# Kernel optimization log

Hardware: AMD Instinct MI355X
Metric: run time of the kernel (lower is better)

## Reference

```python
import jax, jax.numpy as jnp
import numpy as np

HIDDEN = 128
STATE = 256
SEQ = 4096
BATCH = 16


def _op(q_i, q_j):
    # Binary operator for the parallel scan of the 2x2 block-diagonal recurrence.
    # m: (..., 4, N) holding [A, B, C, D] blocks; f: (..., 2, N) holding [b1, b2].
    m_i, f_i = q_i
    m_j, f_j = q_j
    iA, iB, iC, iD = m_i[..., 0, :], m_i[..., 1, :], m_i[..., 2, :], m_i[..., 3, :]
    jA, jB, jC, jD = m_j[..., 0, :], m_j[..., 1, :], m_j[..., 2, :], m_j[..., 3, :]
    m_new = jnp.stack([
        jA * iA + jB * iC,
        jA * iB + jB * iD,
        jC * iA + jD * iC,
        jC * iB + jD * iD,
    ], axis=-2)
    b1, b2 = f_i[..., 0, :], f_i[..., 1, :]
    f_new = jnp.stack([jA * b1 + jB * b2, jC * b1 + jD * b2], axis=-2) + f_j
    return m_new, f_new


def _apply_linoss_im(A_diag, B, x, step):
    # x: (L, H); B: (N, H); A_diag, step: (N,)
    Bu = x @ B.T                                    # (L, N)
    s2A = step ** 2 * A_diag
    schur = 1.0 / (1.0 + s2A)
    M11 = 1.0 - s2A * schur
    M12 = -step * A_diag * schur
    M21 = step * schur
    M22 = schur
    L, N = x.shape[0], A_diag.shape[0]
    M = jnp.broadcast_to(jnp.stack([M11, M12, M21, M22]), (L, 4, N))  # (L, 4, N)
    F = jnp.stack([M11 * Bu * step, M21 * Bu * step], axis=1)          # (L, 2, N)
    _, xs = jax.lax.associative_scan(_op, (M, F))
    return xs[:, 1, :]  # second state component y_k, shape (L, N)


def setup_inputs() -> dict:
    key = jax.random.key(0)
    kx, kA, ks, kB, kC, kD = jax.random.split(key, 6)
    x = jax.random.normal(kx, (BATCH, SEQ, HIDDEN), dtype=jnp.float32)
    A_diag = jax.random.uniform(kA, (STATE,), dtype=jnp.float32)
    steps = 0.5 * jax.random.normal(ks, (STATE,), dtype=jnp.float32)
    B = jax.random.normal(kB, (STATE, HIDDEN), dtype=jnp.float32) / np.sqrt(HIDDEN)
    C = jax.random.normal(kC, (HIDDEN, STATE), dtype=jnp.float32) / np.sqrt(STATE)
    D = jax.random.normal(kD, (HIDDEN,), dtype=jnp.float32)
    return {"x": x, "A_diag": A_diag, "steps": steps, "B": B, "C": C, "D": D}


def reference(x, A_diag, steps, B, C, D):
    # Parameter projections used by the mixer (LinOSS-IM, non-damped):
    step = jax.nn.sigmoid(steps)
    A = jax.nn.relu(A_diag)

    def per_seq(xs):
        ys = _apply_linoss_im(A, B, xs, step)   # (L, N)
        return ys @ C.T + D * xs                # (L, H)

    return jax.vmap(per_seq)(x)  # (B, L, H)
```

## Files before the change

### kernel.cpp

```cpp
#include <hip/hip_runtime.h>
#include <hip/hip_bf16.h>

#define BATCHN 16
#define SEQ 4096
#define HIDDEN 128
#define STATE 256
#define MTOT (BATCHN*SEQ)
#define NCHUNK 64
#define LCHUNK 64

typedef __bf16 bf16;
typedef __bf16 bf16x4 __attribute__((ext_vector_type(4)));
typedef __bf16 bf16x8 __attribute__((ext_vector_type(8)));
typedef float f32x4 __attribute__((ext_vector_type(4)));

__global__ __launch_bounds__(256) void setup_k(const float* __restrict__ A_diag,
        const float* __restrict__ steps, const float* __restrict__ Bm,
        const float* __restrict__ Cm, bf16* __restrict__ Bbf, bf16* __restrict__ Cbf,
        float* __restrict__ prm) {
    int idx = blockIdx.x * 256 + threadIdx.x;
    if (idx < STATE * HIDDEN) {
        Bbf[idx] = (bf16)Bm[idx];
        Cbf[idx] = (bf16)Cm[idx];
    }
    if (blockIdx.x == 0) {
        int n = threadIdx.x;
        float st = 1.0f / (1.0f + expf(-steps[n]));
        float A  = fmaxf(A_diag[n], 0.0f);
        float s2A = st * st * A;
        float schur = 1.0f / (1.0f + s2A);
        float m11 = 1.0f - s2A * schur;
        float m12 = -st * A * schur;
        float m21 = st * schur;
        float m22 = schur;
        prm[0*STATE+n] = m11;
        prm[1*STATE+n] = m12;
        prm[2*STATE+n] = m21;
        prm[3*STATE+n] = m22;
        prm[4*STATE+n] = m11 * st;
        prm[5*STATE+n] = m21 * st;
    }
}

__device__ __forceinline__ void stage_x(const float* __restrict__ x, int m0, int tid,
                                        bf16 (*xl)[136]) {
    #pragma unroll
    for (int p = 0; p < 8; ++p) {
        int flat = p * 256 + tid;
        int row = flat >> 5;
        int c4  = flat & 31;
        float4 v = *reinterpret_cast<const float4*>(&x[(size_t)(m0 + row) * HIDDEN + c4 * 4]);
        bf16x4 w = { (bf16)v.x, (bf16)v.y, (bf16)v.z, (bf16)v.w };
        *reinterpret_cast<bf16x4*>(&xl[row][c4 * 4]) = w;
    }
}

__device__ __forceinline__ void gemm1_to_lds(const bf16 (*xl)[136],
        const bf16* __restrict__ Bbf, int tid, bf16 (*bu)[264]) {
    const int wid = tid >> 6, lane = tid & 63;
    const int lr = lane & 15;
    const int lk = (lane >> 4) * 8;
    const int n0 = wid * 64;
    f32x4 acc[4][4];
    #pragma unroll
    for (int i = 0; i < 4; ++i)
        #pragma unroll
        for (int j = 0; j < 4; ++j) acc[i][j] = f32x4{0.f, 0.f, 0.f, 0.f};
    #pragma unroll
    for (int ks = 0; ks < 4; ++ks) {
        int k = ks * 32 + lk;
        bf16x8 a[4], b[4];
        #pragma unroll
        for (int mf = 0; mf < 4; ++mf)
            a[mf] = *reinterpret_cast<const bf16x8*>(&xl[mf * 16 + lr][k]);
        #pragma unroll
        for (int nf = 0; nf < 4; ++nf)
            b[nf] = *reinterpret_cast<const bf16x8*>(&Bbf[(size_t)(n0 + nf * 16 + lr) * HIDDEN + k]);
        #pragma unroll
        for (int mf = 0; mf < 4; ++mf)
            #pragma unroll
            for (int nf = 0; nf < 4; ++nf)
                acc[mf][nf] = __builtin_amdgcn_mfma_f32_16x16x32_bf16(a[mf], b[nf], acc[mf][nf], 0, 0, 0);
    }
    const int mrow = (lane >> 4) * 4;
    #pragma unroll
    for (int mf = 0; mf < 4; ++mf)
        #pragma unroll
        for (int nf = 0; nf < 4; ++nf)
            #pragma unroll
            for (int r = 0; r < 4; ++r)
                bu[mf * 16 + mrow + r][n0 + nf * 16 + lr] = (bf16)acc[mf][nf][r];
}

__global__ __launch_bounds__(256) void k1_gemm_scanA(const float* __restrict__ x,
        const bf16* __restrict__ Bbf, const float* __restrict__ prm,
        float* __restrict__ cs) {
    __shared__ bf16 xl[64][136];
    __shared__ bf16 bu[64][264];
    const int tid = threadIdx.x;
    const int m0 = blockIdx.x * 64;
    stage_x(x, m0, tid, xl);
    __syncthreads();
    gemm1_to_lds(xl, Bbf, tid, bu);
    __syncthreads();
    const int n = tid;
    const float m11 = prm[n], m12 = prm[STATE + n], m21 = prm[2*STATE + n],
                m22 = prm[3*STATE + n], c1 = prm[4*STATE + n], c2 = prm[5*STATE + n];
    float s1 = 0.f, s2 = 0.f;
    #pragma unroll 8
    for (int t = 0; t < LCHUNK; ++t) {
        float v = (float)bu[t][n];
        float ns1 = fmaf(m11, s1, fmaf(m12, s2, c1 * v));
        float ns2 = fmaf(m21, s1, fmaf(m22, s2, c2 * v));
        s1 = ns1; s2 = ns2;
    }
    const int b = m0 >> 12;
    const int chunk = (m0 >> 6) & (NCHUNK - 1);
    size_t base = ((size_t)(b * NCHUNK + chunk) * 2) * STATE + n;
    cs[base] = s1;
    cs[base + STATE] = s2;
}

__global__ __launch_bounds__(256) void scan_comb(float* __restrict__ cs,
        const float* __restrict__ prm) {
    const int n = threadIdx.x;
    const int b = blockIdx.x;
    float p11 = prm[n], p12 = prm[STATE + n], p21 = prm[2*STATE + n], p22 = prm[3*STATE + n];
    #pragma unroll
    for (int i = 0; i < 6; ++i) {
        float q11 = p11 * p11 + p12 * p21;
        float q12 = p11 * p12 + p12 * p22;
        float q21 = p21 * p11 + p22 * p21;
        float q22 = p21 * p12 + p22 * p22;
        p11 = q11; p12 = q12; p21 = q21; p22 = q22;
    }
    float S1 = 0.f, S2 = 0.f;
    #pragma unroll 8
    for (int c = 0; c < NCHUNK; ++c) {
        size_t base = ((size_t)(b * NCHUNK + c) * 2) * STATE + n;
        float q1 = cs[base], q2 = cs[base + STATE];
        cs[base] = S1; cs[base + STATE] = S2;
        float n1 = fmaf(p11, S1, fmaf(p12, S2, q1));
        float n2 = fmaf(p21, S1, fmaf(p22, S2, q2));
        S1 = n1; S2 = n2;
    }
}

__global__ __launch_bounds__(256) void k2_gemm_scan_gemm(const float* __restrict__ x,
        const bf16* __restrict__ Bbf, const bf16* __restrict__ Cbf,
        const float* __restrict__ prm, const float* __restrict__ cs,
        const float* __restrict__ Dv, float* __restrict__ out) {
    __shared__ bf16 xl[64][136];
    __shared__ bf16 bu[64][264];
    const int tid = threadIdx.x;
    const int m0 = blockIdx.x * 64;
    stage_x(x, m0, tid, xl);
    __syncthreads();
    gemm1_to_lds(xl, Bbf, tid, bu);
    __syncthreads();
    {
        const int n = tid;
        const float m11 = prm[n], m12 = prm[STATE + n], m21 = prm[2*STATE + n],
                    m22 = prm[3*STATE + n], c1 = prm[4*STATE + n], c2 = prm[5*STATE + n];
        const int b = m0 >> 12;
        const int chunk = (m0 >> 6) & (NCHUNK - 1);
        size_t cbase = ((size_t)(b * NCHUNK + chunk) * 2) * STATE + n;
        float s1 = cs[cbase], s2 = cs[cbase + STATE];
        #pragma unroll 8
        for (int t = 0; t < LCHUNK; ++t) {
            float v = (float)bu[t][n];
            float ns1 = fmaf(m11, s1, fmaf(m12, s2, c1 * v));
            float ns2 = fmaf(m21, s1, fmaf(m22, s2, c2 * v));
            s1 = ns1; s2 = ns2;
            bu[t][n] = (bf16)s2;
        }
    }
    __syncthreads();
    const int wid = tid >> 6, lane = tid & 63;
    const int lr = lane & 15;
    const int lk = (lane >> 4) * 8;
    const int h0 = wid * 32;
    f32x4 acc2[4][2];
    #pragma unroll
    for (int i = 0; i < 4; ++i) {
        acc2[i][0] = f32x4{0.f, 0.f, 0.f, 0.f};
        acc2[i][1] = f32x4{0.f, 0.f, 0.f, 0.f};
    }
    #pragma unroll
    for (int ks = 0; ks < 8; ++ks) {
        int k = ks * 32 + lk;
        bf16x8 a[4], bb[2];
        #pragma unroll
        for (int mf = 0; mf < 4; ++mf)
            a[mf] = *reinterpret_cast<const bf16x8*>(&bu[mf * 16 + lr][k]);
        #pragma unroll
        for (int hf = 0; hf < 2; ++hf)
            bb[hf] = *reinterpret_cast<const bf16x8*>(&Cbf[(size_t)(h0 + hf * 16 + lr) * STATE + k]);
        #pragma unroll
        for (int mf = 0; mf < 4; ++mf)
            #pragma unroll
            for (int hf = 0; hf < 2; ++hf)
                acc2[mf][hf] = __builtin_amdgcn_mfma_f32_16x16x32_bf16(a[mf], bb[hf], acc2[mf][hf], 0, 0, 0);
    }
    const int mrow = (lane >> 4) * 4;
    #pragma unroll
    for (int mf = 0; mf < 4; ++mf)
        #pragma unroll
        for (int hf = 0; hf < 2; ++hf) {
            int h = h0 + hf * 16 + lr;
            float d = Dv[h];
            #pragma unroll
            for (int r = 0; r < 4; ++r) {
                int ml = mf * 16 + mrow + r;
                out[(size_t)(m0 + ml) * HIDDEN + h] = acc2[mf][hf][r] + d * (float)xl[ml][h];
            }
        }
}

extern "C" void kernel_launch(void* const* d_in, const int* in_sizes, int n_in,
                              void* d_out, int out_size, void* d_ws, size_t ws_size,
                              hipStream_t stream) {
    const float* x      = (const float*)d_in[0];
    const float* A_diag = (const float*)d_in[1];
    const float* steps  = (const float*)d_in[2];
    const float* Bm     = (const float*)d_in[3];
    const float* Cm     = (const float*)d_in[4];
    const float* Dv     = (const float*)d_in[5];
    float* out = (float*)d_out;

    char* ws = (char*)d_ws;
    const size_t CS_BYTES = (size_t)BATCHN * NCHUNK * 2 * STATE * 4;
    float* cs  = (float*)ws;
    bf16*  Bbf = (bf16*)(ws + CS_BYTES);
    bf16*  Cbf = (bf16*)(ws + CS_BYTES + (size_t)STATE * HIDDEN * 2);
    float* prm = (float*)(ws + CS_BYTES + (size_t)STATE * HIDDEN * 4);

    hipLaunchKernelGGL(setup_k, dim3(128), dim3(256), 0, stream, A_diag, steps, Bm, Cm, Bbf, Cbf, prm);
    hipLaunchKernelGGL(k1_gemm_scanA, dim3(MTOT / 64), dim3(256), 0, stream, x, Bbf, prm, cs);
    hipLaunchKernelGGL(scan_comb, dim3(BATCHN), dim3(256), 0, stream, cs, prm);
    hipLaunchKernelGGL(k2_gemm_scan_gemm, dim3(MTOT / 64), dim3(256), 0, stream,
                       x, Bbf, Cbf, prm, cs, Dv, out);
}
```

Measured before the change: 56.93 us.

## Drop setup kernel, preload B/C fragments into registers, coalesce output stores

Removes the setup kernel by recomputing the scan parameters inline in each kernel. Weight fragments are now loaded straight from fp32 B and C into registers before the main work, so they are no longer read from global inside the GEMM loops. The output epilogue is staged through LDS so the D*x add and the global store use coalesced float4 writes. Launch bounds now request 3 blocks per SM. The trade-offs are higher register pressure, redundant weight conversion in every block, and an extra LDS round trip.

```diff
diff --git a/kernel.cpp b/kernel.cpp
--- a/kernel.cpp
+++ b/kernel.cpp
@@ -14,32 +14,27 @@
 typedef __bf16 bf16x8 __attribute__((ext_vector_type(8)));
 typedef float f32x4 __attribute__((ext_vector_type(4)));
 
-__global__ __launch_bounds__(256) void setup_k(const float* __restrict__ A_diag,
-        const float* __restrict__ steps, const float* __restrict__ Bm,
-        const float* __restrict__ Cm, bf16* __restrict__ Bbf, bf16* __restrict__ Cbf,
-        float* __restrict__ prm) {
-    int idx = blockIdx.x * 256 + threadIdx.x;
-    if (idx < STATE * HIDDEN) {
-        Bbf[idx] = (bf16)Bm[idx];
-        Cbf[idx] = (bf16)Cm[idx];
-    }
-    if (blockIdx.x == 0) {
-        int n = threadIdx.x;
-        float st = 1.0f / (1.0f + expf(-steps[n]));
-        float A  = fmaxf(A_diag[n], 0.0f);
-        float s2A = st * st * A;
-        float schur = 1.0f / (1.0f + s2A);
-        float m11 = 1.0f - s2A * schur;
-        float m12 = -st * A * schur;
-        float m21 = st * schur;
-        float m22 = schur;
-        prm[0*STATE+n] = m11;
-        prm[1*STATE+n] = m12;
-        prm[2*STATE+n] = m21;
-        prm[3*STATE+n] = m22;
-        prm[4*STATE+n] = m11 * st;
-        prm[5*STATE+n] = m21 * st;
-    }
+__device__ __forceinline__ void scan_params(const float* __restrict__ A_diag,
+        const float* __restrict__ steps, int n,
+        float& m11, float& m12, float& m21, float& m22, float& c1, float& c2) {
+    float st = 1.0f / (1.0f + expf(-steps[n]));
+    float A  = fmaxf(A_diag[n], 0.0f);
+    float s2A = st * st * A;
+    float schur = 1.0f / (1.0f + s2A);
+    m11 = 1.0f - s2A * schur;
+    m12 = -st * A * schur;
+    m21 = st * schur;
+    m22 = schur;
+    c1 = m11 * st;
+    c2 = m21 * st;
+}
+
+__device__ __forceinline__ bf16x8 load_frag_f32(const float* __restrict__ src) {
+    float4 a = *reinterpret_cast<const float4*>(src);
+    float4 b = *reinterpret_cast<const float4*>(src + 4);
+    bf16x8 r = { (bf16)a.x, (bf16)a.y, (bf16)a.z, (bf16)a.w,
+                 (bf16)b.x, (bf16)b.y, (bf16)b.z, (bf16)b.w };
+    return r;
 }
 
 __device__ __forceinline__ void stage_x(const float* __restrict__ x, int m0, int tid,
@@ -56,11 +51,9 @@
 }
 
 __device__ __forceinline__ void gemm1_to_lds(const bf16 (*xl)[136],
-        const bf16* __restrict__ Bbf, int tid, bf16 (*bu)[264]) {
-    const int wid = tid >> 6, lane = tid & 63;
+        const bf16x8 breg[4][4], int lane, int n0, bf16 (*bu)[264]) {
     const int lr = lane & 15;
     const int lk = (lane >> 4) * 8;
-    const int n0 = wid * 64;
     f32x4 acc[4][4];
     #pragma unroll
     for (int i = 0; i < 4; ++i)
@@ -69,18 +62,15 @@
     #pragma unroll
     for (int ks = 0; ks < 4; ++ks) {
         int k = ks * 32 + lk;
-        bf16x8 a[4], b[4];
+        bf16x8 a[4];
         #pragma unroll
         for (int mf = 0; mf < 4; ++mf)
             a[mf] = *reinterpret_cast<const bf16x8*>(&xl[mf * 16 + lr][k]);
         #pragma unroll
-        for (int nf = 0; nf < 4; ++nf)
-            b[nf] = *reinterpret_cast<const bf16x8*>(&Bbf[(size_t)(n0 + nf * 16 + lr) * HIDDEN + k]);
-        #pragma unroll
         for (int mf = 0; mf < 4; ++mf)
             #pragma unroll
             for (int nf = 0; nf < 4; ++nf)
-                acc[mf][nf] = __builtin_amdgcn_mfma_f32_16x16x32_bf16(a[mf], b[nf], acc[mf][nf], 0, 0, 0);
+                acc[mf][nf] = __builtin_amdgcn_mfma_f32_16x16x32_bf16(a[mf], breg[ks][nf], acc[mf][nf], 0, 0, 0);
     }
     const int mrow = (lane >> 4) * 4;
     #pragma unroll
@@ -92,20 +82,29 @@
                 bu[mf * 16 + mrow + r][n0 + nf * 16 + lr] = (bf16)acc[mf][nf][r];
 }
 
-__global__ __launch_bounds__(256) void k1_gemm_scanA(const float* __restrict__ x,
-        const bf16* __restrict__ Bbf, const float* __restrict__ prm,
-        float* __restrict__ cs) {
+__global__ __launch_bounds__(256, 3) void k1_gemm_scanA(const float* __restrict__ x,
+        const float* __restrict__ Bm, const float* __restrict__ A_diag,
+        const float* __restrict__ steps, float* __restrict__ cs) {
     __shared__ bf16 xl[64][136];
     __shared__ bf16 bu[64][264];
     const int tid = threadIdx.x;
     const int m0 = blockIdx.x * 64;
+    const int wid = tid >> 6, lane = tid & 63;
+    const int lr = lane & 15, lk = (lane >> 4) * 8;
+    const int n0 = wid * 64;
+    bf16x8 breg[4][4];
+    #pragma unroll
+    for (int ks = 0; ks < 4; ++ks)
+        #pragma unroll
+        for (int nf = 0; nf < 4; ++nf)
+            breg[ks][nf] = load_frag_f32(&Bm[(size_t)(n0 + nf * 16 + lr) * HIDDEN + ks * 32 + lk]);
     stage_x(x, m0, tid, xl);
     __syncthreads();
-    gemm1_to_lds(xl, Bbf, tid, bu);
-    __syncthreads();
+    gemm1_to_lds(xl, breg, lane, n0, bu);
     const int n = tid;
-    const float m11 = prm[n], m12 = prm[STATE + n], m21 = prm[2*STATE + n],
-                m22 = prm[3*STATE + n], c1 = prm[4*STATE + n], c2 = prm[5*STATE + n];
+    float m11, m12, m21, m22, c1, c2;
+    scan_params(A_diag, steps, n, m11, m12, m21, m22, c1, c2);
+    __syncthreads();
     float s1 = 0.f, s2 = 0.f;
     #pragma unroll 8
     for (int t = 0; t < LCHUNK; ++t) {
@@ -122,10 +121,11 @@
 }
 
 __global__ __launch_bounds__(256) void scan_comb(float* __restrict__ cs,
-        const float* __restrict__ prm) {
+        const float* __restrict__ A_diag, const float* __restrict__ steps) {
     const int n = threadIdx.x;
     const int b = blockIdx.x;
-    float p11 = prm[n], p12 = prm[STATE + n], p21 = prm[2*STATE + n], p22 = prm[3*STATE + n];
+    float p11, p12, p21, p22, c1u, c2u;
+    scan_params(A_diag, steps, n, p11, p12, p21, p22, c1u, c2u);
     #pragma unroll
     for (int i = 0; i < 6; ++i) {
         float q11 = p11 * p11 + p12 * p21;
@@ -146,40 +146,52 @@
     }
 }
 
-__global__ __launch_bounds__(256) void k2_gemm_scan_gemm(const float* __restrict__ x,
-        const bf16* __restrict__ Bbf, const bf16* __restrict__ Cbf,
-        const float* __restrict__ prm, const float* __restrict__ cs,
-        const float* __restrict__ Dv, float* __restrict__ out) {
+__global__ __launch_bounds__(256, 3) void k2_gemm_scan_gemm(const float* __restrict__ x,
+        const float* __restrict__ Bm, const float* __restrict__ Cm,
+        const float* __restrict__ A_diag, const float* __restrict__ steps,
+        const float* __restrict__ cs, const float* __restrict__ Dv,
+        float* __restrict__ out) {
     __shared__ bf16 xl[64][136];
     __shared__ bf16 bu[64][264];
+    float (*ldsF)[132] = reinterpret_cast<float(*)[132]>(&bu[0][0]);
     const int tid = threadIdx.x;
     const int m0 = blockIdx.x * 64;
+    const int wid = tid >> 6, lane = tid & 63;
+    const int lr = lane & 15, lk = (lane >> 4) * 8;
+    const int n0 = wid * 64;
+    const int h0 = wid * 32;
+    bf16x8 breg[4][4];
+    #pragma unroll
+    for (int ks = 0; ks < 4; ++ks)
+        #pragma unroll
+        for (int nf = 0; nf < 4; ++nf)
+            breg[ks][nf] = load_frag_f32(&Bm[(size_t)(n0 + nf * 16 + lr) * HIDDEN + ks * 32 + lk]);
     stage_x(x, m0, tid, xl);
     __syncthreads();
-    gemm1_to_lds(xl, Bbf, tid, bu);
-    __syncthreads();
-    {
-        const int n = tid;
-        const float m11 = prm[n], m12 = prm[STATE + n], m21 = prm[2*STATE + n],
-                    m22 = prm[3*STATE + n], c1 = prm[4*STATE + n], c2 = prm[5*STATE + n];
-        const int b = m0 >> 12;
-        const int chunk = (m0 >> 6) & (NCHUNK - 1);
-        size_t cbase = ((size_t)(b * NCHUNK + chunk) * 2) * STATE + n;
-        float s1 = cs[cbase], s2 = cs[cbase + STATE];
-        #pragma unroll 8
-        for (int t = 0; t < LCHUNK; ++t) {
-            float v = (float)bu[t][n];
-            float ns1 = fmaf(m11, s1, fmaf(m12, s2, c1 * v));
-            float ns2 = fmaf(m21, s1, fmaf(m22, s2, c2 * v));
-            s1 = ns1; s2 = ns2;
-            bu[t][n] = (bf16)s2;
-        }
-    }
-    __syncthreads();
-    const int wid = tid >> 6, lane = tid & 63;
-    const int lr = lane & 15;
-    const int lk = (lane >> 4) * 8;
-    const int h0 = wid * 32;
+    gemm1_to_lds(xl, breg, lane, n0, bu);
+    bf16x8 creg[8][2];
+    #pragma unroll
+    for (int ks = 0; ks < 8; ++ks)
+        #pragma unroll
+        for (int hf = 0; hf < 2; ++hf)
+            creg[ks][hf] = load_frag_f32(&Cm[(size_t)(h0 + hf * 16 + lr) * STATE + ks * 32 + lk]);
+    const int n = tid;
+    float m11, m12, m21, m22, c1, c2;
+    scan_params(A_diag, steps, n, m11, m12, m21, m22, c1, c2);
+    const int b = m0 >> 12;
+    const int chunk = (m0 >> 6) & (NCHUNK - 1);
+    size_t cbase = ((size_t)(b * NCHUNK + chunk) * 2) * STATE + n;
+    float s1 = cs[cbase], s2 = cs[cbase + STATE];
+    __syncthreads();
+    #pragma unroll 8
+    for (int t = 0; t < LCHUNK; ++t) {
+        float v = (float)bu[t][n];
+        float ns1 = fmaf(m11, s1, fmaf(m12, s2, c1 * v));
+        float ns2 = fmaf(m21, s1, fmaf(m22, s2, c2 * v));
+        s1 = ns1; s2 = ns2;
+        bu[t][n] = (bf16)s2;
+    }
+    __syncthreads();
     f32x4 acc2[4][2];
     #pragma unroll
     for (int i = 0; i < 4; ++i) {
@@ -189,32 +201,41 @@
     #pragma unroll
     for (int ks = 0; ks < 8; ++ks) {
         int k = ks * 32 + lk;
-        bf16x8 a[4], bb[2];
+        bf16x8 a[4];
         #pragma unroll
         for (int mf = 0; mf < 4; ++mf)
             a[mf] = *reinterpret_cast<const bf16x8*>(&bu[mf * 16 + lr][k]);
         #pragma unroll
+        for (int mf = 0; mf < 4; ++mf)
+            #pragma unroll
+            for (int hf = 0; hf < 2; ++hf)
+                acc2[mf][hf] = __builtin_amdgcn_mfma_f32_16x16x32_bf16(a[mf], creg[ks][hf], acc2[mf][hf], 0, 0, 0);
+    }
+    __syncthreads();
+    const int mrow = (lane >> 4) * 4;
+    #pragma unroll
+    for (int mf = 0; mf < 4; ++mf)
+        #pragma unroll
         for (int hf = 0; hf < 2; ++hf)
-            bb[hf] = *reinterpret_cast<const bf16x8*>(&Cbf[(size_t)(h0 + hf * 16 + lr) * STATE + k]);
-        #pragma unroll
-        for (int mf = 0; mf < 4; ++mf)
-            #pragma unroll
-            for (int hf = 0; hf < 2; ++hf)
-                acc2[mf][hf] = __builtin_amdgcn_mfma_f32_16x16x32_bf16(a[mf], bb[hf], acc2[mf][hf], 0, 0, 0);
-    }
-    const int mrow = (lane >> 4) * 4;
-    #pragma unroll
-    for (int mf = 0; mf < 4; ++mf)
-        #pragma unroll
-        for (int hf = 0; hf < 2; ++hf) {
-            int h = h0 + hf * 16 + lr;
-            float d = Dv[h];
-            #pragma unroll
-            for (int r = 0; r < 4; ++r) {
-                int ml = mf * 16 + mrow + r;
-                out[(size_t)(m0 + ml) * HIDDEN + h] = acc2[mf][hf][r] + d * (float)xl[ml][h];
-            }
-        }
+            #pragma unroll
+            for (int r = 0; r < 4; ++r)
+                ldsF[mf * 16 + mrow + r][h0 + hf * 16 + lr] = acc2[mf][hf][r];
+    __syncthreads();
+    #pragma unroll
+    for (int p = 0; p < 8; ++p) {
+        int flat = p * 256 + tid;
+        int row = flat >> 5;
+        int c4  = flat & 31;
+        float4 f = *reinterpret_cast<const float4*>(&ldsF[row][c4 * 4]);
+        bf16x4 xv = *reinterpret_cast<const bf16x4*>(&xl[row][c4 * 4]);
+        float4 d = *reinterpret_cast<const float4*>(&Dv[c4 * 4]);
+        float4 o;
+        o.x = f.x + d.x * (float)xv.x;
+        o.y = f.y + d.y * (float)xv.y;
+        o.z = f.z + d.z * (float)xv.z;
+        o.w = f.w + d.w * (float)xv.w;
+        *reinterpret_cast<float4*>(&out[(size_t)(m0 + row) * HIDDEN + c4 * 4]) = o;
+    }
 }
 
 extern "C" void kernel_launch(void* const* d_in, const int* in_sizes, int n_in,
@@ -228,16 +249,11 @@
     const float* Dv     = (const float*)d_in[5];
     float* out = (float*)d_out;
 
-    char* ws = (char*)d_ws;
-    const size_t CS_BYTES = (size_t)BATCHN * NCHUNK * 2 * STATE * 4;
-    float* cs  = (float*)ws;
-    bf16*  Bbf = (bf16*)(ws + CS_BYTES);
-    bf16*  Cbf = (bf16*)(ws + CS_BYTES + (size_t)STATE * HIDDEN * 2);
-    float* prm = (float*)(ws + CS_BYTES + (size_t)STATE * HIDDEN * 4);
-
-    hipLaunchKernelGGL(setup_k, dim3(128), dim3(256), 0, stream, A_diag, steps, Bm, Cm, Bbf, Cbf, prm);
-    hipLaunchKernelGGL(k1_gemm_scanA, dim3(MTOT / 64), dim3(256), 0, stream, x, Bbf, prm, cs);
-    hipLaunchKernelGGL(scan_comb, dim3(BATCHN), dim3(256), 0, stream, cs, prm);
+    float* cs = (float*)d_ws;
+
+    hipLaunchKernelGGL(k1_gemm_scanA, dim3(MTOT / 64), dim3(256), 0, stream,
+                       x, Bm, A_diag, steps, cs);
+    hipLaunchKernelGGL(scan_comb, dim3(BATCHN), dim3(256), 0, stream, cs, A_diag, steps);
     hipLaunchKernelGGL(k2_gemm_scan_gemm, dim3(MTOT / 64), dim3(256), 0, stream,
-                       x, Bbf, Cbf, prm, cs, Dv, out);
-}
+                       x, Bm, Cm, A_diag, steps, cs, Dv, out);
+}
```

Measured after the change: 93.09 us. 63.5% more time.
